# Optimization experiments

Hardware: AMD Instinct MI355X
Metric: run time of the kernel (lower is better)

Reference implementation:

```python
import jax, jax.numpy as jnp
import numpy as np

HEADS = 8
DIM_HEAD = 64
MAX_REL = 200  # max_rel_dist


def setup_inputs() -> dict:
    key = jax.random.key(0)
    ks = jax.random.split(key, 5)
    B, N, D = 4, 2048, 512
    x = jax.random.normal(ks[0], (B, N, D), dtype=jnp.float32)
    temporal_mask = jax.random.randint(ks[1], (N, N), 0, 2, dtype=jnp.int32)
    gamma = jnp.ones((D,), jnp.float32)
    beta = jnp.zeros((D,), jnp.float32)
    Wqkv = jax.random.normal(ks[2], (D, 3 * HEADS * DIM_HEAD), dtype=jnp.float32) * 0.02
    Wout = jax.random.normal(ks[3], (HEADS * DIM_HEAD, D), dtype=jnp.float32) * 0.02
    bout = jnp.zeros((D,), jnp.float32)
    rel_table = jax.random.normal(ks[4], (2 * MAX_REL - 1,), dtype=jnp.float32) * 0.02
    return {"x": x, "gamma": gamma, "beta": beta, "Wqkv": Wqkv, "Wout": Wout,
            "bout": bout, "rel_table": rel_table, "temporal_mask": temporal_mask}


def reference(x, gamma, beta, Wqkv, Wout, bout, rel_table, temporal_mask):
    B, N, D = x.shape
    scale = DIM_HEAD ** -0.5
    # LayerNorm
    mu = jnp.mean(x, axis=-1, keepdims=True)
    var = jnp.mean(jnp.square(x - mu), axis=-1, keepdims=True)
    xn = (x - mu) * jax.lax.rsqrt(var + 1e-5) * gamma + beta
    # QKV projection (no bias), split heads: b n (h d) -> b h n d
    qkv = xn @ Wqkv  # [B, N, 3*H*d]
    q, k, v = jnp.split(qkv, 3, axis=-1)
    split = lambda t: t.reshape(B, N, HEADS, DIM_HEAD).transpose(0, 2, 1, 3)
    q, k, v = split(q), split(k), split(v)
    # scores with learned relative-position bias
    dots = jnp.einsum('bhnd,bhmd->bhnm', q, k) * scale  # [B,H,N,N]
    idx = jnp.arange(N)
    rel = jnp.clip(idx[:, None] - idx[None, :], -(MAX_REL - 1), MAX_REL - 1) + MAX_REL - 1
    dots = dots + rel_table[rel][None, None, :, :]
    # temporal mask (0 -> -inf); large negative for grad safety
    dots = jnp.where(temporal_mask[None, None, :, :] == 0, jnp.float32(-1e9), dots)
    attn = jax.nn.softmax(dots, axis=-1)
    out = jnp.einsum('bhnm,bhmd->bhnd', attn, v)
    out = out.transpose(0, 2, 1, 3).reshape(B, N, HEADS * DIM_HEAD)
    return out @ Wout + bout
```

## Files before the change

kernel.cpp:

```cpp
#include <hip/hip_runtime.h>

typedef __attribute__((ext_vector_type(8))) short bf16x8;
typedef __attribute__((ext_vector_type(4))) short bf16x4;
typedef __attribute__((ext_vector_type(4))) float f32x4;
typedef unsigned short ushort_t;

#define B_ 4
#define H_ 8
#define N_ 2048
#define D_ 512
#define MAXREL 199
#define LOG2E 1.4426950408889634f

__device__ __forceinline__ ushort_t f2bf(float f) {
    union { float f; unsigned u; } v; v.f = f;
    unsigned r = v.u + 0x7fffu + ((v.u >> 16) & 1u);
    return (ushort_t)(r >> 16);
}
__device__ __forceinline__ float bf2f(ushort_t u) {
    union { unsigned u; float f; } v; v.u = ((unsigned)u) << 16;
    return v.f;
}
__device__ __forceinline__ float fexp2(float x) {
#if __has_builtin(__builtin_amdgcn_exp2f)
    return __builtin_amdgcn_exp2f(x);
#else
    return __expf(x * 0.6931471805599453f);
#endif
}
__device__ __forceinline__ unsigned cvt_pk_bf16(float lo, float hi) {
    unsigned r;
    asm("v_cvt_pk_bf16_f32 %0, %1, %2" : "=v"(r) : "v"(lo), "v"(hi));
    return r;
}
__device__ __forceinline__ void gl_lds16(const ushort_t* g, ushort_t* l) {
    __builtin_amdgcn_global_load_lds(
        (const __attribute__((address_space(1))) void*)g,
        (__attribute__((address_space(3))) void*)l,
        16, 0, 0);
}

#define PREP_BIAS  512
#define PREP_LN    2048
#define PREP_WQ    768
#define PREP_WO    256
__global__ __launch_bounds__(256) void prep_kernel(const float* __restrict__ x,
                                                   const float* __restrict__ gamma,
                                                   const float* __restrict__ beta,
                                                   ushort_t* __restrict__ xn,
                                                   const float* __restrict__ Wqkv,
                                                   ushort_t* __restrict__ WqkvT,
                                                   const float* __restrict__ Wout,
                                                   ushort_t* __restrict__ WoutT,
                                                   const float* __restrict__ rel,
                                                   const int* __restrict__ mask,
                                                   ushort_t* __restrict__ bp) {
    __shared__ float smem[32 * 33];
    const int blk = blockIdx.x;
    const int t = threadIdx.x;

    if (blk < PREP_BIAS) {
        const int base = blk * 8192;
        #pragma unroll
        for (int p = 0; p < 8; p++) {
            int idx = base + p * 1024 + t * 4;
            int n = idx >> 11, m = idx & 2047;
            const int4 mv = *(const int4*)&mask[idx];
            union { ushort_t us[4]; unsigned long long ll; } pkv;
            #pragma unroll
            for (int j = 0; j < 4; j++) {
                int dl = n - (m + j);
                dl = dl < -MAXREL ? -MAXREL : (dl > MAXREL ? MAXREL : dl);
                int mj = (j == 0) ? mv.x : (j == 1) ? mv.y : (j == 2) ? mv.z : mv.w;
                float v = (mj == 0) ? -1e9f : rel[dl + MAXREL] * LOG2E;
                pkv.us[j] = f2bf(v);
            }
            int off = ((n >> 7) << 18) + ((m >> 6) << 13) + (((n >> 4) & 7) << 10)
                    + (((m >> 4) & 3) << 8) + (((m >> 2) & 3) << 6) + ((n & 15) << 2);
            *(unsigned long long*)(bp + off) = pkv.ll;
        }
    } else if (blk < PREP_BIAS + PREP_LN) {
        const int row = (blk - PREP_BIAS) * 4 + (t >> 6);
        const int l = t & 63;
        const float* xr = x + (size_t)row * D_;
        float4 a = *(const float4*)&xr[l * 4];
        float4 c = *(const float4*)&xr[256 + l * 4];
        float s = (a.x + a.y) + (a.z + a.w) + (c.x + c.y) + (c.z + c.w);
        #pragma unroll
        for (int o = 1; o < 64; o <<= 1) s += __shfl_xor(s, o);
        float mu = s * (1.0f / D_);
        float dx0 = a.x - mu, dx1 = a.y - mu, dx2 = a.z - mu, dx3 = a.w - mu;
        float dy0 = c.x - mu, dy1 = c.y - mu, dy2 = c.z - mu, dy3 = c.w - mu;
        float s2 = dx0*dx0 + dx1*dx1 + dx2*dx2 + dx3*dx3
                 + dy0*dy0 + dy1*dy1 + dy2*dy2 + dy3*dy3;
        #pragma unroll
        for (int o = 1; o < 64; o <<= 1) s2 += __shfl_xor(s2, o);
        float rs = rsqrtf(s2 * (1.0f / D_) + 1e-5f);
        float4 g1 = *(const float4*)&gamma[l * 4];
        float4 g2 = *(const float4*)&gamma[256 + l * 4];
        float4 b1 = *(const float4*)&beta[l * 4];
        float4 b2 = *(const float4*)&beta[256 + l * 4];
        ushort_t* yr = xn + (size_t)row * D_;
        union { ushort_t us[4]; unsigned long long ll; } o1, o2;
        o1.us[0] = f2bf(dx0 * rs * g1.x + b1.x);
        o1.us[1] = f2bf(dx1 * rs * g1.y + b1.y);
        o1.us[2] = f2bf(dx2 * rs * g1.z + b1.z);
        o1.us[3] = f2bf(dx3 * rs * g1.w + b1.w);
        o2.us[0] = f2bf(dy0 * rs * g2.x + b2.x);
        o2.us[1] = f2bf(dy1 * rs * g2.y + b2.y);
        o2.us[2] = f2bf(dy2 * rs * g2.z + b2.z);
        o2.us[3] = f2bf(dy3 * rs * g2.w + b2.w);
        *(unsigned long long*)(yr + l * 4) = o1.ll;
        *(unsigned long long*)(yr + 256 + l * 4) = o2.ll;
    } else {
        const float* W; ushort_t* Wt; int Nn, i;
        if (blk < PREP_BIAS + PREP_LN + PREP_WQ) {
            i = blk - (PREP_BIAS + PREP_LN); W = Wqkv; Wt = WqkvT; Nn = 1536;
        } else {
            i = blk - (PREP_BIAS + PREP_LN + PREP_WQ); W = Wout; Wt = WoutT; Nn = 512;
        }
        const int nb = Nn >> 5;
        const int bx = (i % nb) * 32, by = (i / nb) * 32;
        const int tx = t & 31, ty = t >> 5;
        float (*tile)[33] = (float(*)[33])smem;
        #pragma unroll
        for (int k = 0; k < 32; k += 8)
            tile[ty + k][tx] = W[(size_t)(by + ty + k) * Nn + bx + tx];
        __syncthreads();
        #pragma unroll
        for (int k = 0; k < 32; k += 8)
            Wt[(size_t)(bx + ty + k) * 512 + by + tx] = f2bf(tile[tx][ty + k]);
    }
}

__global__ __launch_bounds__(256) void gemm_qkv(const ushort_t* __restrict__ A,
                                                const ushort_t* __restrict__ Bt,
                                                ushort_t* __restrict__ qb,
                                                ushort_t* __restrict__ kb,
                                                ushort_t* __restrict__ vb) {
    __shared__ ushort_t SH[8192];
    ushort_t* As = SH;
    ushort_t* Bs = SH + 4096;
    const int t = threadIdx.x;
    const int lane = t & 63, w = t >> 6;
    const int m16 = lane & 15, quad = lane >> 4;
    const int wr = w >> 1, wc = w & 1;
    const int r0 = blockIdx.y * 128, c0 = blockIdx.x * 128;

    const ushort_t* Ag = A  + (size_t)(r0 + (t >> 2)) * D_ + (t & 3) * 8;
    const ushort_t* Bg = Bt + (size_t)(c0 + (t >> 2)) * D_ + (t & 3) * 8;
    ushort_t* AsW = As + w * 512;
    ushort_t* BsW = Bs + w * 512;

    f32x4 acc[4][4];
    #pragma unroll
    for (int i = 0; i < 4; i++)
        #pragma unroll
        for (int j = 0; j < 4; j++) acc[i][j] = (f32x4){0.f, 0.f, 0.f, 0.f};

    for (int k0 = 0; k0 < D_; k0 += 32) {
        gl_lds16(Ag + k0, AsW);
        gl_lds16(Ag + k0 + (size_t)64 * D_, AsW + 2048);
        gl_lds16(Bg + k0, BsW);
        gl_lds16(Bg + k0 + (size_t)64 * D_, BsW + 2048);
        __syncthreads();
        bf16x8 af[4], bfr[4];
        #pragma unroll
        for (int rt = 0; rt < 4; rt++)
            af[rt] = *(const bf16x8*)(As + (wr * 64 + rt * 16 + m16) * 32 + quad * 8);
        #pragma unroll
        for (int ct = 0; ct < 4; ct++)
            bfr[ct] = *(const bf16x8*)(Bs + (wc * 64 + ct * 16 + m16) * 32 + quad * 8);
        #pragma unroll
        for (int rt = 0; rt < 4; rt++)
            #pragma unroll
            for (int ct = 0; ct < 4; ct++)
                acc[rt][ct] = __builtin_amdgcn_mfma_f32_16x16x32_bf16(af[rt], bfr[ct], acc[rt][ct], 0, 0, 0);
        __syncthreads();
    }

    const int b_blk = r0 >> 11, n_base = r0 & 2047;
    #pragma unroll
    for (int ph = 0; ph < 2; ph++) {
        const int cph = c0 + ph * 64;
        const int which = cph >> 9;
        const int h = (cph >> 6) & 7;
        if (ph) __syncthreads();
        if (wc == ph) {
            if (which != 2) {
                const float sc = (which == 0) ? (0.125f * LOG2E) : 1.0f;
                #pragma unroll
                for (int ct = 0; ct < 4; ct++) {
                    int dcol = ct * 16 + m16;
                    #pragma unroll
                    for (int rt = 0; rt < 4; rt++)
                        #pragma unroll
                        for (int r = 0; r < 4; r++) {
                            int nl = wr * 64 + rt * 16 + quad * 4 + r;
                            SH[nl * 64 + (dcol ^ ((nl & 7) << 3))] = f2bf(acc[rt][ct][r] * sc);
                        }
                }
            } else {
                #pragma unroll
                for (int ct = 0; ct < 4; ct++) {
                    int dcol = ct * 16 + m16;
                    #pragma unroll
                    for (int rt = 0; rt < 4; rt++) {
                        int nl = wr * 64 + rt * 16 + quad * 4;
                        union { ushort_t us[4]; unsigned long long ll; } pkv;
                        #pragma unroll
                        for (int r = 0; r < 4; r++) pkv.us[r] = f2bf(acc[rt][ct][r]);
                        *(unsigned long long*)(&SH[dcol * 128 + (nl ^ ((dcol & 7) << 3))]) = pkv.ll;
                    }
                }
            }
        }
        __syncthreads();
        if (which != 2) {
            ushort_t* dst = (which == 0) ? qb : kb;
            #pragma unroll
            for (int p = 0; p < 4; p++) {
                int nl = p * 32 + (t >> 3);
                int d0 = (t & 7) * 8;
                bf16x8 vv = *(const bf16x8*)&SH[nl * 64 + (d0 ^ ((nl & 7) << 3))];
                *(bf16x8*)(dst + ((size_t)(b_blk * H_ + h) * N_ + n_base + nl) * 64 + d0) = vv;
            }
        } else {
            #pragma unroll
            for (int p = 0; p < 4; p++) {
                int dr = p * 16 + (t >> 4);
                int n0 = (t & 15) * 8;
                bf16x8 vv = *(const bf16x8*)&SH[dr * 128 + (n0 ^ ((dr & 7) << 3))];
                *(bf16x8*)(vb + ((size_t)(b_blk * H_ + h) * 64 + dr) * N_ + n_base + n0) = vv;
            }
        }
    }
}

__global__ __launch_bounds__(256) void gemm_out(const ushort_t* __restrict__ A,
                                                const ushort_t* __restrict__ Bt,
                                                const float* __restrict__ bias,
                                                float* __restrict__ C) {
    __shared__ ushort_t As[64 * 32];
    __shared__ ushort_t Bs[128 * 32];
    const int t = threadIdx.x;
    const int lane = t & 63, w = t >> 6;
    const int m16 = lane & 15, quad = lane >> 4;
    const int wr = w >> 1, wc = w & 1;
    const int r0 = blockIdx.y * 64, c0 = blockIdx.x * 128;

    const ushort_t* Ag = A  + (size_t)(r0 + (t >> 2)) * D_ + (t & 3) * 8;
    const ushort_t* Bg = Bt + (size_t)(c0 + (t >> 2)) * D_ + (t & 3) * 8;
    ushort_t* AsW = As + w * 512;
    ushort_t* BsW = Bs + w * 512;

    f32x4 acc[2][4];
    #pragma unroll
    for (int i = 0; i < 2; i++)
        #pragma unroll
        for (int j = 0; j < 4; j++) acc[i][j] = (f32x4){0.f, 0.f, 0.f, 0.f};

    for (int k0 = 0; k0 < D_; k0 += 32) {
        gl_lds16(Ag + k0, AsW);
        gl_lds16(Bg + k0, BsW);
        gl_lds16(Bg + k0 + (size_t)64 * D_, BsW + 2048);
        __syncthreads();
        bf16x8 af[2], bfr[4];
        #pragma unroll
        for (int mf = 0; mf < 2; mf++)
            af[mf] = *(const bf16x8*)(As + (wr * 32 + mf * 16 + m16) * 32 + quad * 8);
        #pragma unroll
        for (int nt = 0; nt < 4; nt++)
            bfr[nt] = *(const bf16x8*)(Bs + (wc * 64 + nt * 16 + m16) * 32 + quad * 8);
        #pragma unroll
        for (int mf = 0; mf < 2; mf++)
            #pragma unroll
            for (int nt = 0; nt < 4; nt++)
                acc[mf][nt] = __builtin_amdgcn_mfma_f32_16x16x32_bf16(af[mf], bfr[nt], acc[mf][nt], 0, 0, 0);
        __syncthreads();
    }

    #pragma unroll
    for (int mf = 0; mf < 2; mf++) {
        #pragma unroll
        for (int nt = 0; nt < 4; nt++) {
            int col = c0 + wc * 64 + nt * 16 + m16;
            int row0 = r0 + wr * 32 + mf * 16 + quad * 4;
            float bv = bias[col];
            #pragma unroll
            for (int r = 0; r < 4; r++)
                C[(size_t)(row0 + r) * 512 + col] = acc[mf][nt][r] + bv;
        }
    }
}

#define ATTN_TILE(JT, KCUR, VCUR, KNXT, VNXT, BCUR, BNXT)                              \
  {                                                                                    \
    const int jt = (JT);                                                               \
    const int buf = jt & 1;                                                            \
    if (jt + 2 < 32) {                                                                 \
      KNXT = *(const bf16x8*)(kgbase + (size_t)((jt + 2) * 64 + srow) * 64 + scb * 8); \
      VNXT = *(const bf16x8*)(vgbase + (size_t)srow * N_ + (jt + 2) * 64 + scb * 8);   \
    }                                                                                  \
    if (jt + 1 < 32) {                                                                 \
      _Pragma("unroll")                                                                \
      for (int nt = 0; nt < 4; nt++)                                                   \
        BNXT[nt] = *(const bf16x4*)(bpb + ((jt + 1) << 13) + (nt << 8));               \
    }                                                                                  \
    unsigned pk[8];                                                                    \
    __builtin_amdgcn_s_setprio(1);                                                     \
    _Pragma("unroll")                                                                  \
    for (int nt = 0; nt < 4; nt++) {                                                   \
      f32x4 a2;                                                                        \
      _Pragma("unroll")                                                                \
      for (int r = 0; r < 4; r++) a2[r] = bf2f((ushort_t)BCUR[nt][r]);                 \
      int kr = nt * 16 + m16;                                                          \
      bf16x8 kf0 = *(const bf16x8*)(&Ks[buf][kr * 64 + ((quad) ^ (kr & 7)) * 8]);      \
      bf16x8 kf1 = *(const bf16x8*)(&Ks[buf][kr * 64 + ((quad + 4) ^ (kr & 7)) * 8]);  \
      a2 = __builtin_amdgcn_mfma_f32_16x16x32_bf16(kf0, qa0, a2, 0, 0, 0);             \
      a2 = __builtin_amdgcn_mfma_f32_16x16x32_bf16(kf1, qa1, a2, 0, 0, 0);             \
      float p0 = fexp2(a2[0]), p1 = fexp2(a2[1]);                                      \
      float p2 = fexp2(a2[2]), p3 = fexp2(a2[3]);                                      \
      rsum += (p0 + p1) + (p2 + p3);                                                   \
      pk[nt * 2]     = cvt_pk_bf16(p0, p1);                                            \
      pk[nt * 2 + 1] = cvt_pk_bf16(p2, p3);                                            \
    }                                                                                  \
    __builtin_amdgcn_s_setprio(0);                                                     \
    _Pragma("unroll")                                                                  \
    for (int i = 0; i < 4; i++) {                                                      \
      int chunk = 2 * i + (quad >> 1);                                                 \
      union { unsigned uu[2]; unsigned long long ll; } wrp;                            \
      wrp.uu[0] = pk[2 * i]; wrp.uu[1] = pk[2 * i + 1];                                \
      *(unsigned long long*)(pw + m16 * 64 + ((chunk ^ (m16 & 7)) << 3)                \
                             + (quad & 1) * 4) = wrp.ll;                               \
    }                                                                                  \
    bf16x8 pa0 = *(const bf16x8*)(pw + m16 * 64 + ((quad ^ (m16 & 7)) << 3));          \
    bf16x8 pa1 = *(const bf16x8*)(pw + m16 * 64 + (((quad + 4) ^ (m16 & 7)) << 3));    \
    __builtin_amdgcn_s_setprio(1);                                                     \
    _Pragma("unroll")                                                                  \
    for (int nt = 0; nt < 4; nt++) {                                                   \
      int d = nt * 16 + m16;                                                           \
      bf16x8 vf0 = *(const bf16x8*)(&Vs[buf][d * 64 + ((quad) ^ (d & 7)) * 8]);        \
      bf16x8 vf1 = *(const bf16x8*)(&Vs[buf][d * 64 + ((quad + 4) ^ (d & 7)) * 8]);    \
      o[nt] = __builtin_amdgcn_mfma_f32_16x16x32_bf16(pa0, vf0, o[nt], 0, 0, 0);       \
      o[nt] = __builtin_amdgcn_mfma_f32_16x16x32_bf16(pa1, vf1, o[nt], 0, 0, 0);       \
    }                                                                                  \
    __builtin_amdgcn_s_setprio(0);                                                     \
    if (jt + 1 < 32) {                                                                 \
      *(bf16x8*)(&Ks[buf ^ 1][soff]) = KCUR;                                           \
      *(bf16x8*)(&Vs[buf ^ 1][soff]) = VCUR;                                           \
    }                                                                                  \
    __syncthreads();                                                                   \
  }

__global__ __launch_bounds__(512, 4) void attn_mfma(const ushort_t* __restrict__ qb,
                                                    const ushort_t* __restrict__ kb,
                                                    const ushort_t* __restrict__ vb,
                                                    const ushort_t* __restrict__ bp,
                                                    ushort_t* __restrict__ attn) {
    __shared__ ushort_t Ks[2][64 * 64];
    __shared__ ushort_t Vs[2][64 * 64];
    __shared__ ushort_t p_s[8][16 * 64];

    const int t = threadIdx.x;
    const int w = t >> 6, lane = t & 63;
    const int m16 = lane & 15, quad = lane >> 4;
    const int id = blockIdx.x;
    const int bh = id & 31;
    const int qt = id >> 5;
    const int b = bh >> 3, h = bh & 7;
    const int n0w = qt * 128 + w * 16;

    const int srow = t >> 3, scb = t & 7;
    const int soff = srow * 64 + (scb ^ (srow & 7)) * 8;
    const ushort_t* kgbase = kb + ((size_t)bh * N_) * 64;
    const ushort_t* vgbase = vb + ((size_t)bh * 64) * N_;

    const ushort_t* qpb = qb + ((size_t)(bh * N_ + n0w + m16)) * 64 + quad * 8;
    bf16x8 qa0 = *(const bf16x8*)(qpb);
    bf16x8 qa1 = *(const bf16x8*)(qpb + 32);

    const ushort_t* bpb = bp + ((size_t)qt << 18) + (w << 10) + (quad << 6) + (m16 << 2);

    *(bf16x8*)(&Ks[0][soff]) = *(const bf16x8*)(kgbase + (size_t)srow * 64 + scb * 8);
    *(bf16x8*)(&Vs[0][soff]) = *(const bf16x8*)(vgbase + (size_t)srow * N_ + scb * 8);
    bf16x8 kA = *(const bf16x8*)(kgbase + (size_t)(64 + srow) * 64 + scb * 8);
    bf16x8 vA = *(const bf16x8*)(vgbase + (size_t)srow * N_ + 64 + scb * 8);
    bf16x8 kB, vB;
    bf16x4 bA[4], bB[4];
    #pragma unroll
    for (int nt = 0; nt < 4; nt++) bA[nt] = *(const bf16x4*)(bpb + (nt << 8));
    __syncthreads();

    f32x4 o[4];
    #pragma unroll
    for (int nt = 0; nt < 4; nt++) o[nt] = (f32x4){0.f, 0.f, 0.f, 0.f};
    float rsum = 0.f;

    ushort_t* pw = p_s[w];

    for (int jt2 = 0; jt2 < 16; jt2++) {
        ATTN_TILE(2 * jt2,     kA, vA, kB, vB, bA, bB);
        ATTN_TILE(2 * jt2 + 1, kB, vB, kA, vA, bB, bA);
    }

    rsum += __shfl_xor(rsum, 16);
    rsum += __shfl_xor(rsum, 32);

    #pragma unroll
    for (int r = 0; r < 4; r++) {
        float inv = 1.0f / __shfl(rsum, quad * 4 + r);
        int n = n0w + quad * 4 + r;
        ushort_t* orow = attn + ((size_t)(b * N_ + n)) * 512 + h * 64 + m16;
        #pragma unroll
        for (int nt = 0; nt < 4; nt++) orow[nt * 16] = f2bf(o[nt][r] * inv);
    }
}

extern "C" void kernel_launch(void* const* d_in, const int* in_sizes, int n_in,
                              void* d_out, int out_size, void* d_ws, size_t ws_size,
                              hipStream_t stream) {
    const float* x     = (const float*)d_in[0];
    const float* gamma = (const float*)d_in[1];
    const float* beta  = (const float*)d_in[2];
    const float* Wqkv  = (const float*)d_in[3];
    const float* Wout  = (const float*)d_in[4];
    const float* bout  = (const float*)d_in[5];
    const float* rel   = (const float*)d_in[6];
    const int*   mask  = (const int*)d_in[7];
    float* out = (float*)d_out;

    char* wsb = (char*)d_ws;
    ushort_t* xn    = (ushort_t*)(wsb);
    ushort_t* attnb = (ushort_t*)(wsb + ( 8u << 20));
    ushort_t* qb    = (ushort_t*)(wsb + (16u << 20));
    ushort_t* kb    = (ushort_t*)(wsb + (24u << 20));
    ushort_t* vb    = (ushort_t*)(wsb + (32u << 20));
    ushort_t* WqkvT = (ushort_t*)(wsb + (40u << 20));
    ushort_t* WoutT = (ushort_t*)(wsb + (42u << 20));
    ushort_t* bp    = (ushort_t*)(wsb + (44u << 20));

    prep_kernel<<<PREP_BIAS + PREP_LN + PREP_WQ + PREP_WO, 256, 0, stream>>>(
        x, gamma, beta, xn, Wqkv, WqkvT, Wout, WoutT, rel, mask, bp);

    gemm_qkv<<<dim3(1536 / 128, 8192 / 128), 256, 0, stream>>>(xn, WqkvT, qb, kb, vb);

    attn_mfma<<<512, 512, 0, stream>>>(qb, kb, vb, bp, attnb);

    gemm_out<<<dim3(512 / 128, 8192 / 64), 256, 0, stream>>>(attnb, WoutT, bout, out);
}
```

Measured before the change: 198.4 us.

## Move bias/mask precompute into QKV GEMM launch and store epilogue directly

The relative-position bias and mask packing work moves from the prep kernel into extra blocks of the QKV GEMM launch, so it runs alongside the GEMM tiles instead of ahead of them. The GEMM epilogue also drops its LDS-staged transpose and writes Q/K/V straight to global memory with scattered 2-byte stores, and 8-byte stores for V. This removes the LDS round trip and barriers, but it gives up coalesced 16-byte stores, which may raise write traffic cost.

After: 194.9 us. No clear change (-1.8%).

```diff
diff --git a/kernel.cpp b/kernel.cpp
--- a/kernel.cpp
+++ b/kernel.cpp
@@ -40,7 +40,6 @@
         16, 0, 0);
 }
 
-#define PREP_BIAS  512
 #define PREP_LN    2048
 #define PREP_WQ    768
 #define PREP_WO    256
@@ -51,36 +50,13 @@
                                                    const float* __restrict__ Wqkv,
                                                    ushort_t* __restrict__ WqkvT,
                                                    const float* __restrict__ Wout,
-                                                   ushort_t* __restrict__ WoutT,
-                                                   const float* __restrict__ rel,
-                                                   const int* __restrict__ mask,
-                                                   ushort_t* __restrict__ bp) {
+                                                   ushort_t* __restrict__ WoutT) {
     __shared__ float smem[32 * 33];
     const int blk = blockIdx.x;
     const int t = threadIdx.x;
 
-    if (blk < PREP_BIAS) {
-        const int base = blk * 8192;
-        #pragma unroll
-        for (int p = 0; p < 8; p++) {
-            int idx = base + p * 1024 + t * 4;
-            int n = idx >> 11, m = idx & 2047;
-            const int4 mv = *(const int4*)&mask[idx];
-            union { ushort_t us[4]; unsigned long long ll; } pkv;
-            #pragma unroll
-            for (int j = 0; j < 4; j++) {
-                int dl = n - (m + j);
-                dl = dl < -MAXREL ? -MAXREL : (dl > MAXREL ? MAXREL : dl);
-                int mj = (j == 0) ? mv.x : (j == 1) ? mv.y : (j == 2) ? mv.z : mv.w;
-                float v = (mj == 0) ? -1e9f : rel[dl + MAXREL] * LOG2E;
-                pkv.us[j] = f2bf(v);
-            }
-            int off = ((n >> 7) << 18) + ((m >> 6) << 13) + (((n >> 4) & 7) << 10)
-                    + (((m >> 4) & 3) << 8) + (((m >> 2) & 3) << 6) + ((n & 15) << 2);
-            *(unsigned long long*)(bp + off) = pkv.ll;
-        }
-    } else if (blk < PREP_BIAS + PREP_LN) {
-        const int row = (blk - PREP_BIAS) * 4 + (t >> 6);
+    if (blk < PREP_LN) {
+        const int row = blk * 4 + (t >> 6);
         const int l = t & 63;
         const float* xr = x + (size_t)row * D_;
         float4 a = *(const float4*)&xr[l * 4];
@@ -114,10 +90,10 @@
         *(unsigned long long*)(yr + 256 + l * 4) = o2.ll;
     } else {
         const float* W; ushort_t* Wt; int Nn, i;
-        if (blk < PREP_BIAS + PREP_LN + PREP_WQ) {
-            i = blk - (PREP_BIAS + PREP_LN); W = Wqkv; Wt = WqkvT; Nn = 1536;
+        if (blk < PREP_LN + PREP_WQ) {
+            i = blk - PREP_LN; W = Wqkv; Wt = WqkvT; Nn = 1536;
         } else {
-            i = blk - (PREP_BIAS + PREP_LN + PREP_WQ); W = Wout; Wt = WoutT; Nn = 512;
+            i = blk - (PREP_LN + PREP_WQ); W = Wout; Wt = WoutT; Nn = 512;
         }
         const int nb = Nn >> 5;
         const int bx = (i % nb) * 32, by = (i / nb) * 32;
@@ -133,19 +109,48 @@
     }
 }
 
+#define QKV_BIAS_BLKS 512
 __global__ __launch_bounds__(256) void gemm_qkv(const ushort_t* __restrict__ A,
                                                 const ushort_t* __restrict__ Bt,
                                                 ushort_t* __restrict__ qb,
                                                 ushort_t* __restrict__ kb,
-                                                ushort_t* __restrict__ vb) {
-    __shared__ ushort_t SH[8192];
-    ushort_t* As = SH;
-    ushort_t* Bs = SH + 4096;
+                                                ushort_t* __restrict__ vb,
+                                                const float* __restrict__ rel,
+                                                const int* __restrict__ mask,
+                                                ushort_t* __restrict__ bp) {
+    const int bid = blockIdx.x;
     const int t = threadIdx.x;
+
+    if (bid < QKV_BIAS_BLKS) {
+        const int base = bid * 8192;
+        #pragma unroll
+        for (int p = 0; p < 8; p++) {
+            int idx = base + p * 1024 + t * 4;
+            int n = idx >> 11, m = idx & 2047;
+            const int4 mv = *(const int4*)&mask[idx];
+            union { ushort_t us[4]; unsigned long long ll; } pkv;
+            #pragma unroll
+            for (int j = 0; j < 4; j++) {
+                int dl = n - (m + j);
+                dl = dl < -MAXREL ? -MAXREL : (dl > MAXREL ? MAXREL : dl);
+                int mj = (j == 0) ? mv.x : (j == 1) ? mv.y : (j == 2) ? mv.z : mv.w;
+                float v = (mj == 0) ? -1e9f : rel[dl + MAXREL] * LOG2E;
+                pkv.us[j] = f2bf(v);
+            }
+            int off = ((n >> 7) << 18) + ((m >> 6) << 13) + (((n >> 4) & 7) << 10)
+                    + (((m >> 4) & 3) << 8) + (((m >> 2) & 3) << 6) + ((n & 15) << 2);
+            *(unsigned long long*)(bp + off) = pkv.ll;
+        }
+        return;
+    }
+
+    __shared__ ushort_t As[128 * 32];
+    __shared__ ushort_t Bs[128 * 32];
+    const int gid = bid - QKV_BIAS_BLKS;
     const int lane = t & 63, w = t >> 6;
     const int m16 = lane & 15, quad = lane >> 4;
     const int wr = w >> 1, wc = w & 1;
-    const int r0 = blockIdx.y * 128, c0 = blockIdx.x * 128;
+    const int r0 = (gid / 12) * 128, c0 = (gid % 12) * 128;
 
     const ushort_t* Ag = A  + (size_t)(r0 + (t >> 2)) * D_ + (t & 3) * 8;
     const ushort_t* Bg = Bt + (size_t)(c0 + (t >> 2)) * D_ + (t & 3) * 8;
@@ -179,59 +184,29 @@
         __syncthreads();
     }
 
-    const int b_blk = r0 >> 11, n_base = r0 & 2047;
-    #pragma unroll
-    for (int ph = 0; ph < 2; ph++) {
-        const int cph = c0 + ph * 64;
-        const int which = cph >> 9;
-        const int h = (cph >> 6) & 7;
-        if (ph) __syncthreads();
-        if (wc == ph) {
-            if (which != 2) {
-                const float sc = (which == 0) ? (0.125f * LOG2E) : 1.0f;
+    #pragma unroll
+    for (int ct = 0; ct < 4; ct++) {
+        int cc = c0 + wc * 64 + ct * 16;
+        int which = cc >> 9;
+        int h = (cc >> 6) & 7;
+        int d = (cc & 63) + m16;
+        #pragma unroll
+        for (int rt = 0; rt < 4; rt++) {
+            int rowb = r0 + wr * 64 + rt * 16 + quad * 4;
+            int b = rowb >> 11, n0 = rowb & 2047;
+            if (which == 0) {
                 #pragma unroll
-                for (int ct = 0; ct < 4; ct++) {
-                    int dcol = ct * 16 + m16;
-                    #pragma unroll
-                    for (int rt = 0; rt < 4; rt++)
-                        #pragma unroll
-                        for (int r = 0; r < 4; r++) {
-                            int nl = wr * 64 + rt * 16 + quad * 4 + r;
-                            SH[nl * 64 + (dcol ^ ((nl & 7) << 3))] = f2bf(acc[rt][ct][r] * sc);
-                        }
-                }
+                for (int r = 0; r < 4; r++)
+                    qb[((size_t)((b * H_ + h) * N_ + n0 + r)) * 64 + d] = f2bf(acc[rt][ct][r] * (0.125f * LOG2E));
+            } else if (which == 1) {
+                #pragma unroll
+                for (int r = 0; r < 4; r++)
+                    kb[((size_t)((b * H_ + h) * N_ + n0 + r)) * 64 + d] = f2bf(acc[rt][ct][r]);
             } else {
+                union { ushort_t u4[4]; unsigned long long ll; } pk;
                 #pragma unroll
-                for (int ct = 0; ct < 4; ct++) {
-                    int dcol = ct * 16 + m16;
-                    #pragma unroll
-                    for (int rt = 0; rt < 4; rt++) {
-                        int nl = wr * 64 + rt * 16 + quad * 4;
-                        union { ushort_t us[4]; unsigned long long ll; } pkv;
-                        #pragma unroll
-                        for (int r = 0; r < 4; r++) pkv.us[r] = f2bf(acc[rt][ct][r]);
-                        *(unsigned long long*)(&SH[dcol * 128 + (nl ^ ((dcol & 7) << 3))]) = pkv.ll;
-                    }
-                }
-            }
-        }
-        __syncthreads();
-        if (which != 2) {
-            ushort_t* dst = (which == 0) ? qb : kb;
-            #pragma unroll
-            for (int p = 0; p < 4; p++) {
-                int nl = p * 32 + (t >> 3);
-                int d0 = (t & 7) * 8;
-                bf16x8 vv = *(const bf16x8*)&SH[nl * 64 + (d0 ^ ((nl & 7) << 3))];
-                *(bf16x8*)(dst + ((size_t)(b_blk * H_ + h) * N_ + n_base + nl) * 64 + d0) = vv;
-            }
-        } else {
-            #pragma unroll
-            for (int p = 0; p < 4; p++) {
-                int dr = p * 16 + (t >> 4);
-                int n0 = (t & 15) * 8;
-                bf16x8 vv = *(const bf16x8*)&SH[dr * 128 + (n0 ^ ((dr & 7) << 3))];
-                *(bf16x8*)(vb + ((size_t)(b_blk * H_ + h) * 64 + dr) * N_ + n_base + n0) = vv;
+                for (int r = 0; r < 4; r++) pk.u4[r] = f2bf(acc[rt][ct][r]);
+                *(unsigned long long*)(vb + ((size_t)((b * H_ + h) * 64 + d)) * N_ + n0) = pk.ll;
             }
         }
     }
@@ -440,10 +415,10 @@
     ushort_t* WoutT = (ushort_t*)(wsb + (42u << 20));
     ushort_t* bp    = (ushort_t*)(wsb + (44u << 20));
 
-    prep_kernel<<<PREP_BIAS + PREP_LN + PREP_WQ + PREP_WO, 256, 0, stream>>>(
-        x, gamma, beta, xn, Wqkv, WqkvT, Wout, WoutT, rel, mask, bp);
-
-    gemm_qkv<<<dim3(1536 / 128, 8192 / 128), 256, 0, stream>>>(xn, WqkvT, qb, kb, vb);
+    prep_kernel<<<PREP_LN + PREP_WQ + PREP_WO, 256, 0, stream>>>(
+        x, gamma, beta, xn, Wqkv, WqkvT, Wout, WoutT);
+
+    gemm_qkv<<<QKV_BIAS_BLKS + 768, 256, 0, stream>>>(xn, WqkvT, qb, kb, vb, rel, mask, bp);
 
     attn_mfma<<<512, 512, 0, stream>>>(qb, kb, vb, bp, attnb);
 
```
